# Kernel tuning notes

Hardware: AMD Instinct MI355X
Metric: run time of the kernel (lower is better)

The kernel has to match this reference:

```python
import jax, jax.numpy as jnp
import numpy as np

LN_EPS = 1e-5  # torch nn.LayerNorm default


def setup_inputs() -> dict:
    key = jax.random.key(0)
    kx, kw = jax.random.split(key)
    T, B, D = 1024, 8, 2048
    x = jax.random.normal(kx, (T, B, D), dtype=jnp.float32)
    c0 = jnp.zeros((B, D), dtype=jnp.float32)
    # Linear(n_embd, 3*n_embd, bias=False) weight: [3D, D], scaled for sane activations
    W = jax.random.normal(kw, (3 * D, D), dtype=jnp.float32) / np.sqrt(D)
    gamma = jnp.ones((D,), dtype=jnp.float32)
    beta = jnp.zeros((D,), dtype=jnp.float32)
    return {"x": x, "c0": c0, "W": W, "gamma": gamma, "beta": beta}


def reference(x, c0, W, gamma, beta):
    # x: [T, B, D], c0: [B, D], W: [3D, D]
    T, B, D = x.shape
    # Projection for all timesteps at once (same math as per-step Linear).
    ufr = jnp.einsum('tbd,ed->tbe', x, W)  # [T, B, 3D]
    u, f, r = jnp.split(ufr, 3, axis=-1)
    f = jax.nn.sigmoid(f)
    r = jax.nn.sigmoid(r)

    def step(c_prev, inp):
        x_t, u_t, f_t, r_t = inp
        c_t = f_t * c_prev + (1.0 - f_t) * u_t
        h_t = r_t * jnp.tanh(c_t) + (1.0 - r_t) * x_t
        return c_t, h_t

    c_T, h = jax.lax.scan(step, c0, (x, u, f, r))  # h: [T, B, D]

    g = jax.nn.gelu(h, approximate=False)  # torch F.gelu default = exact erf
    mean = jnp.mean(g, axis=-1, keepdims=True)
    var = jnp.var(g, axis=-1, keepdims=True)
    out = (g - mean) * jax.lax.rsqrt(var + LN_EPS) * gamma + beta
    return out, c_T
```

## Files before the change

kernel.cpp:

```cpp
#include <hip/hip_runtime.h>
#include <hip/hip_bf16.h>

#define T_DIM 1024
#define B_DIM 8
#define D_DIM 2048
#define E_DIM 6144
#define N_ROWS 8192
#define K_DIM 2048
#define LN_EPS 1e-5f

#define S2  128
#define CH2 8
#define BD (B_DIM * D_DIM)

typedef short bf16x8 __attribute__((ext_vector_type(8)));
typedef float f32x4 __attribute__((ext_vector_type(4)));

__device__ __forceinline__ unsigned short f2bf(float f) {
  unsigned u = __float_as_uint(f);
  u += 0x7fffu + ((u >> 16) & 1u);
  return (unsigned short)(u >> 16);
}
__device__ __forceinline__ float bf2f(unsigned short h) {
  return __uint_as_float(((unsigned)h) << 16);
}
__device__ __forceinline__ float fast_sigmoid(float x) {
  return __builtin_amdgcn_rcpf(1.f + __expf(-x));
}
__device__ __forceinline__ float fast_tanh(float x) {
  return 1.f - 2.f * __builtin_amdgcn_rcpf(__expf(2.f * x) + 1.f);
}

__global__ __launch_bounds__(256) void cvt2_kernel(
    const float* __restrict__ src0, unsigned short* __restrict__ dst0, int n0,
    const float* __restrict__ src1, unsigned short* __restrict__ dst1, int n1) {
  int i = blockIdx.x * 256 + threadIdx.x;
  const float* s;
  unsigned short* d;
  if (i < n0) {
    s = src0; d = dst0;
  } else {
    i -= n0;
    if (i >= n1) return;
    s = src1; d = dst1;
  }
  float4 v = reinterpret_cast<const float4*>(s)[i];
  ushort4 o;
  o.x = f2bf(v.x); o.y = f2bf(v.y); o.z = f2bf(v.z); o.w = f2bf(v.w);
  reinterpret_cast<ushort4*>(d)[i] = o;
}

#define NT2 32

__global__ __launch_bounds__(512, 2) void gemm8_kernel(
    const unsigned short* __restrict__ A,
    const unsigned short* __restrict__ Bw,
    unsigned short* __restrict__ C) {
  extern __shared__ __align__(16) char smem[];
  const int tid  = threadIdx.x;
  const int lane = tid & 63;
  const int wave = tid >> 6;
  const int wm = wave >> 2;
  const int wn = wave & 3;

  const int bid = blockIdx.x;
  const int tileM = ((bid & 7) * 4 + ((bid >> 3) & 3)) * 256;
  const int tileN = (bid >> 5) * 256;

  const int p0i = wave * 2048 + lane * 16;
  const int p1i = p0i + 1024;
  const int q0i = p0i ^ (((p0i >> 9) & 1) << 5);
  const int q1i = p1i ^ (((p1i >> 9) & 1) << 5);
  const int go0 = ((q0i >> 6) & 127) * 4096 + ((q0i >> 13) << 6) + (q0i & 63);
  const int go1 = ((q1i >> 6) & 127) * 4096 + ((q1i >> 13) << 6) + (q1i & 63);
  const char* Ab = (const char*)A + (size_t)tileM * 4096;
  const char* Bb = (const char*)Bw + (size_t)tileN * 4096;

#define STAGE(kt, h, bufOff)                                                 \
  {                                                                          \
    const char* gs_ = ((h) < 2 ? Ab : Bb) +                                  \
                      (size_t)(((h) & 1) * 128) * 4096 + (size_t)(kt) * 128; \
    char* ds_ = smem + (bufOff) + (h) * 16384 + wave * 2048;                 \
    __builtin_amdgcn_global_load_lds(                                        \
        (const __attribute__((address_space(1))) void*)(gs_ + go0),          \
        (__attribute__((address_space(3))) void*)ds_, 16, 0, 0);             \
    __builtin_amdgcn_global_load_lds(                                        \
        (const __attribute__((address_space(1))) void*)(gs_ + go1),          \
        (__attribute__((address_space(3))) void*)(ds_ + 1024), 16, 0, 0);    \
  }

  const int xbit = ((lane >> 3) & 1) << 5;
  const int aBase = wm * 16384 +
                    (((lane & 15) * 64 + (lane >> 4) * 16) ^ xbit);
  const int bBase = 32768 + (wn >> 1) * 16384 +
                    ((((wn & 1) * 64 + (lane & 15)) * 64 + (lane >> 4) * 16) ^ xbit);

#define RDA(m, bufOff)                                                          \
  a[m][0] = *reinterpret_cast<const bf16x8*>(smem + (bufOff) + aBase + (m) * 1024);        \
  a[m][1] = *reinterpret_cast<const bf16x8*>(smem + (bufOff) + aBase + (m) * 1024 + 8192);
#define RDB(n, bufOff)                                                          \
  b[n][0] = *reinterpret_cast<const bf16x8*>(smem + (bufOff) + bBase + (n) * 1024);        \
  b[n][1] = *reinterpret_cast<const bf16x8*>(smem + (bufOff) + bBase + (n) * 1024 + 8192);
#define MM(m, n)                                                                \
  acc[m][n] = __builtin_amdgcn_mfma_f32_16x16x32_bf16(a[m][0], b[n][0], acc[m][n], 0, 0, 0); \
  acc[m][n] = __builtin_amdgcn_mfma_f32_16x16x32_bf16(a[m][1], b[n][1], acc[m][n], 0, 0, 0);

  bf16x8 a[8][2], b[4][2];
  f32x4 acc[8][4] = {};

  STAGE(0, 0, 0); STAGE(0, 1, 0); STAGE(0, 2, 0); STAGE(0, 3, 0);
  STAGE(1, 0, 65536); STAGE(1, 1, 65536);
  asm volatile("s_waitcnt vmcnt(4)" ::: "memory");
  __builtin_amdgcn_s_barrier();
  RDA(0, 0); RDA(1, 0); RDA(2, 0); RDA(3, 0);
  RDB(0, 0); RDB(1, 0);

  for (int j = 0; j < NT2; ++j) {
    const int buf  = (j & 1) << 16;
    const int nbuf = buf ^ 65536;
    asm volatile("s_waitcnt lgkmcnt(0)" ::: "memory");
    __builtin_amdgcn_s_setprio(1);
    if (j < NT2 - 1) STAGE(j + 1, 2, nbuf);
    RDA(4, buf); RDA(5, buf); RDA(6, buf); RDA(7, buf);
    MM(0, 0); MM(0, 1); MM(1, 0); MM(1, 1);
    MM(2, 0); MM(2, 1); MM(3, 0); MM(3, 1);
    __builtin_amdgcn_s_setprio(0);
    __builtin_amdgcn_s_barrier();
    asm volatile("s_waitcnt lgkmcnt(0)" ::: "memory");
    __builtin_amdgcn_s_setprio(1);
    if (j < NT2 - 1) STAGE(j + 1, 3, nbuf);
    RDB(2, buf); RDB(3, buf);
    MM(4, 0); MM(4, 1); MM(5, 0); MM(5, 1);
    MM(6, 0); MM(6, 1); MM(7, 0); MM(7, 1);
    __builtin_amdgcn_s_setprio(0);
    __builtin_amdgcn_s_barrier();
    asm volatile("s_waitcnt lgkmcnt(0)" ::: "memory");
    __builtin_amdgcn_s_setprio(1);
    if (j < NT2 - 2) STAGE(j + 2, 0, buf);
    MM(0, 2); MM(0, 3); MM(1, 2); MM(1, 3);
    MM(2, 2); MM(2, 3); MM(3, 2); MM(3, 3);
    __builtin_amdgcn_s_setprio(0);
    __builtin_amdgcn_s_barrier();
    if (j < NT2 - 2) {
      STAGE(j + 2, 1, buf);
      asm volatile("s_waitcnt vmcnt(4)" ::: "memory");
    } else if (j == NT2 - 2) {
      asm volatile("s_waitcnt vmcnt(0)" ::: "memory");
    }
    __builtin_amdgcn_s_barrier();
    __builtin_amdgcn_s_setprio(1);
    RDA(0, nbuf); RDA(1, nbuf); RDA(2, nbuf); RDA(3, nbuf);
    RDB(0, nbuf); RDB(1, nbuf);
    MM(4, 2); MM(4, 3); MM(5, 2); MM(5, 3);
    MM(6, 2); MM(6, 3); MM(7, 2); MM(7, 3);
    __builtin_amdgcn_s_setprio(0);
    __builtin_amdgcn_s_barrier();
  }

  const int crow = (lane >> 4) * 4;
  const int ccol = lane & 15;
#pragma unroll
  for (int m = 0; m < 8; ++m) {
#pragma unroll
    for (int n = 0; n < 4; ++n) {
#pragma unroll
      for (int jj = 0; jj < 4; ++jj) {
        int row = tileM + wm * 128 + m * 16 + crow + jj;
        int col = tileN + wn * 64 + n * 16 + ccol;
        C[(size_t)row * E_DIM + col] = f2bf(acc[m][n][jj]);
      }
    }
  }
#undef STAGE
#undef RDA
#undef RDB
#undef MM
}

__global__ __launch_bounds__(256) void scan_p1_kernel(
    const unsigned short* __restrict__ ufr,
    unsigned short* __restrict__ Aout, unsigned short* __restrict__ Bout) {
  const int idx4 = blockIdx.x * 256 + threadIdx.x;
  const int s = blockIdx.y;
  const int b = idx4 >> 9;
  const int d = (idx4 & 511) * 4;
  const unsigned short* up =
      ufr + ((size_t)(s * CH2) * B_DIM + b) * E_DIM + d;
  float A0 = 1.f, A1 = 1.f, A2 = 1.f, A3 = 1.f;
  float Bv0 = 0.f, Bv1 = 0.f, Bv2 = 0.f, Bv3 = 0.f;
#pragma unroll
  for (int it = 0; it < CH2; ++it) {
    ushort4 uv = *(const ushort4*)up;
    ushort4 fv = *(const ushort4*)(up + D_DIM);
    float f0 = fast_sigmoid(bf2f(fv.x));
    float f1 = fast_sigmoid(bf2f(fv.y));
    float f2 = fast_sigmoid(bf2f(fv.z));
    float f3 = fast_sigmoid(bf2f(fv.w));
    A0 *= f0; Bv0 = f0 * Bv0 + (1.f - f0) * bf2f(uv.x);
    A1 *= f1; Bv1 = f1 * Bv1 + (1.f - f1) * bf2f(uv.y);
    A2 *= f2; Bv2 = f2 * Bv2 + (1.f - f2) * bf2f(uv.z);
    A3 *= f3; Bv3 = f3 * Bv3 + (1.f - f3) * bf2f(uv.w);
    up += (size_t)B_DIM * E_DIM;
  }
  size_t o = (size_t)s * BD + b * D_DIM + d;
  ushort4 ao = {f2bf(A0), f2bf(A1), f2bf(A2), f2bf(A3)};
  ushort4 bo = {f2bf(Bv0), f2bf(Bv1), f2bf(Bv2), f2bf(Bv3)};
  *(ushort4*)(Aout + o) = ao;
  *(ushort4*)(Bout + o) = bo;
}

__global__ __launch_bounds__(64) void scan_p2_kernel(
    const float* __restrict__ c0,
    const unsigned short* __restrict__ Ain, const unsigned short* __restrict__ Bin,
    unsigned short* __restrict__ cs, float* __restrict__ cT) {
  const int idx = blockIdx.x * 64 + threadIdx.x;
  float c = c0[idx];
  for (int s = 0; s < S2; ++s) {
    cs[(size_t)s * BD + idx] = f2bf(c);
    c = bf2f(Ain[(size_t)s * BD + idx]) * c + bf2f(Bin[(size_t)s * BD + idx]);
  }
  cT[idx] = c;
}

__global__ __launch_bounds__(256) void scan_p3ln_kernel(
    const unsigned short* __restrict__ xb,
    const unsigned short* __restrict__ ufr,
    const unsigned short* __restrict__ csb,
    const float* __restrict__ gamma,
    const float* __restrict__ beta,
    float* __restrict__ out) {
  const int b = blockIdx.x & (B_DIM - 1);
  const int s = blockIdx.x >> 3;
  const int tid = threadIdx.x;
  const int lane = tid & 63;
  const int wave = tid >> 6;
  const int d0 = tid * 8;
  __shared__ float red[8];

  float c[8];
  {
    const unsigned short* csp = csb + (size_t)s * BD + b * D_DIM + d0;
    ushort4 v0 = *(const ushort4*)csp;
    ushort4 v1 = *(const ushort4*)(csp + 4);
    c[0]=bf2f(v0.x); c[1]=bf2f(v0.y); c[2]=bf2f(v0.z); c[3]=bf2f(v0.w);
    c[4]=bf2f(v1.x); c[5]=bf2f(v1.y); c[6]=bf2f(v1.z); c[7]=bf2f(v1.w);
  }
  float gam[8], bet[8];
  {
    float4 g0 = *(const float4*)(gamma + d0);
    float4 g1 = *(const float4*)(gamma + d0 + 4);
    float4 b0 = *(const float4*)(beta + d0);
    float4 b1 = *(const float4*)(beta + d0 + 4);
    gam[0]=g0.x; gam[1]=g0.y; gam[2]=g0.z; gam[3]=g0.w;
    gam[4]=g1.x; gam[5]=g1.y; gam[6]=g1.z; gam[7]=g1.w;
    bet[0]=b0.x; bet[1]=b0.y; bet[2]=b0.z; bet[3]=b0.w;
    bet[4]=b1.x; bet[5]=b1.y; bet[6]=b1.z; bet[7]=b1.w;
  }

  for (int it = 0; it < CH2; ++it) {
    const size_t rowo = (size_t)(s * CH2 + it) * B_DIM + b;
    const unsigned short* up = ufr + rowo * E_DIM + d0;
    const unsigned short* xp = xb + rowo * D_DIM + d0;
    ushort4 uv0 = *(const ushort4*)up;
    ushort4 uv1 = *(const ushort4*)(up + 4);
    ushort4 fv0 = *(const ushort4*)(up + D_DIM);
    ushort4 fv1 = *(const ushort4*)(up + D_DIM + 4);
    ushort4 rv0 = *(const ushort4*)(up + 2 * D_DIM);
    ushort4 rv1 = *(const ushort4*)(up + 2 * D_DIM + 4);
    ushort4 xv0 = *(const ushort4*)xp;
    ushort4 xv1 = *(const ushort4*)(xp + 4);
    unsigned short uu[8] = {uv0.x, uv0.y, uv0.z, uv0.w, uv1.x, uv1.y, uv1.z, uv1.w};
    unsigned short ff[8] = {fv0.x, fv0.y, fv0.z, fv0.w, fv1.x, fv1.y, fv1.z, fv1.w};
    unsigned short rr[8] = {rv0.x, rv0.y, rv0.z, rv0.w, rv1.x, rv1.y, rv1.z, rv1.w};
    unsigned short xx[8] = {xv0.x, xv0.y, xv0.z, xv0.w, xv1.x, xv1.y, xv1.z, xv1.w};

    float g[8];
    float s1 = 0.f, sq = 0.f;
#pragma unroll
    for (int jj = 0; jj < 8; ++jj) {
      float f = fast_sigmoid(bf2f(ff[jj]));
      float r = fast_sigmoid(bf2f(rr[jj]));
      c[jj] = f * c[jj] + (1.f - f) * bf2f(uu[jj]);
      float h = r * fast_tanh(c[jj]) + (1.f - r) * bf2f(xx[jj]);
      float gg = 0.5f * h * (1.f + erff(h * 0.70710678118654752f));
      g[jj] = gg;
      s1 += gg;
      sq += gg * gg;
    }
#pragma unroll
    for (int off = 32; off; off >>= 1) {
      s1 += __shfl_xor(s1, off);
      sq += __shfl_xor(sq, off);
    }
    if (lane == 0) { red[wave] = s1; red[4 + wave] = sq; }
    __syncthreads();
    float S1 = red[0] + red[1] + red[2] + red[3];
    float Sq = red[4] + red[5] + red[6] + red[7];
    __syncthreads();
    float mean = S1 * (1.f / D_DIM);
    float var  = Sq * (1.f / D_DIM) - mean * mean;
    float inv = rsqrtf(var + LN_EPS);

    float* op = out + rowo * D_DIM + d0;
    float4 o0 = {(g[0] - mean) * inv * gam[0] + bet[0],
                 (g[1] - mean) * inv * gam[1] + bet[1],
                 (g[2] - mean) * inv * gam[2] + bet[2],
                 (g[3] - mean) * inv * gam[3] + bet[3]};
    float4 o1 = {(g[4] - mean) * inv * gam[4] + bet[4],
                 (g[5] - mean) * inv * gam[5] + bet[5],
                 (g[6] - mean) * inv * gam[6] + bet[6],
                 (g[7] - mean) * inv * gam[7] + bet[7]};
    *(float4*)op = o0;
    *(float4*)(op + 4) = o1;
  }
}

extern "C" void kernel_launch(void* const* d_in, const int* in_sizes, int n_in,
                              void* d_out, int out_size, void* d_ws, size_t ws_size,
                              hipStream_t stream) {
  const float* x     = (const float*)d_in[0];
  const float* c0    = (const float*)d_in[1];
  const float* W     = (const float*)d_in[2];
  const float* gamma = (const float*)d_in[3];
  const float* beta  = (const float*)d_in[4];
  float* out = (float*)d_out;
  float* cT  = out + (size_t)N_ROWS * D_DIM;

  unsigned short* ufr = (unsigned short*)d_ws;
  unsigned short* xb  = ufr + (size_t)N_ROWS * E_DIM;
  unsigned short* wb  = xb + (size_t)N_ROWS * K_DIM;

  unsigned short* Abuf = wb;
  unsigned short* Bbuf = Abuf + (size_t)S2 * BD;
  unsigned short* csb  = Bbuf + (size_t)S2 * BD;

  int nx4 = N_ROWS * K_DIM / 4;
  int nw4 = E_DIM * K_DIM / 4;
  cvt2_kernel<<<(nx4 + nw4 + 255) / 256, 256, 0, stream>>>(x, xb, nx4, W, wb, nw4);

  (void)hipFuncSetAttribute((const void*)gemm8_kernel,
                            hipFuncAttributeMaxDynamicSharedMemorySize, 131072);
  gemm8_kernel<<<768, 512, 131072, stream>>>(xb, wb, ufr);

  dim3 sg(BD / 4 / 256, S2);
  scan_p1_kernel<<<sg, 256, 0, stream>>>(ufr, Abuf, Bbuf);
  scan_p2_kernel<<<BD / 64, 64, 0, stream>>>(c0, Abuf, Bbuf, csb, cT);
  scan_p3ln_kernel<<<B_DIM * S2, 256, 0, stream>>>(xb, ufr, csb, gamma, beta, out);
}
```

Baseline: 266.9 us.

## Widen memory accesses to 16-byte vectors and software-pipeline scan pass-2 loads

```diff
diff --git a/kernel.cpp b/kernel.cpp
--- a/kernel.cpp
+++ b/kernel.cpp
@@ -14,6 +14,7 @@
 #define BD (B_DIM * D_DIM)
 
 typedef short bf16x8 __attribute__((ext_vector_type(8)));
+typedef unsigned short u16x8 __attribute__((ext_vector_type(8)));
 typedef float f32x4 __attribute__((ext_vector_type(4)));
 
 __device__ __forceinline__ unsigned short f2bf(float f) {
@@ -44,10 +45,12 @@
     if (i >= n1) return;
     s = src1; d = dst1;
   }
-  float4 v = reinterpret_cast<const float4*>(s)[i];
-  ushort4 o;
-  o.x = f2bf(v.x); o.y = f2bf(v.y); o.z = f2bf(v.z); o.w = f2bf(v.w);
-  reinterpret_cast<ushort4*>(d)[i] = o;
+  float4 v0 = reinterpret_cast<const float4*>(s)[i * 2];
+  float4 v1 = reinterpret_cast<const float4*>(s)[i * 2 + 1];
+  u16x8 o;
+  o[0] = f2bf(v0.x); o[1] = f2bf(v0.y); o[2] = f2bf(v0.z); o[3] = f2bf(v0.w);
+  o[4] = f2bf(v1.x); o[5] = f2bf(v1.y); o[6] = f2bf(v1.z); o[7] = f2bf(v1.w);
+  *reinterpret_cast<u16x8*>(d + (size_t)i * 8) = o;
 }
 
 #define NT2 32
@@ -180,33 +183,33 @@
 __global__ __launch_bounds__(256) void scan_p1_kernel(
     const unsigned short* __restrict__ ufr,
     unsigned short* __restrict__ Aout, unsigned short* __restrict__ Bout) {
-  const int idx4 = blockIdx.x * 256 + threadIdx.x;
+  const int idx8 = blockIdx.x * 256 + threadIdx.x;
   const int s = blockIdx.y;
-  const int b = idx4 >> 9;
-  const int d = (idx4 & 511) * 4;
+  const int b = idx8 >> 8;
+  const int d = (idx8 & 255) * 8;
   const unsigned short* up =
       ufr + ((size_t)(s * CH2) * B_DIM + b) * E_DIM + d;
-  float A0 = 1.f, A1 = 1.f, A2 = 1.f, A3 = 1.f;
-  float Bv0 = 0.f, Bv1 = 0.f, Bv2 = 0.f, Bv3 = 0.f;
+  float Av[8], Bv[8];
+#pragma unroll
+  for (int q = 0; q < 8; ++q) { Av[q] = 1.f; Bv[q] = 0.f; }
 #pragma unroll
   for (int it = 0; it < CH2; ++it) {
-    ushort4 uv = *(const ushort4*)up;
-    ushort4 fv = *(const ushort4*)(up + D_DIM);
-    float f0 = fast_sigmoid(bf2f(fv.x));
-    float f1 = fast_sigmoid(bf2f(fv.y));
-    float f2 = fast_sigmoid(bf2f(fv.z));
-    float f3 = fast_sigmoid(bf2f(fv.w));
-    A0 *= f0; Bv0 = f0 * Bv0 + (1.f - f0) * bf2f(uv.x);
-    A1 *= f1; Bv1 = f1 * Bv1 + (1.f - f1) * bf2f(uv.y);
-    A2 *= f2; Bv2 = f2 * Bv2 + (1.f - f2) * bf2f(uv.z);
-    A3 *= f3; Bv3 = f3 * Bv3 + (1.f - f3) * bf2f(uv.w);
+    u16x8 uv = *reinterpret_cast<const u16x8*>(up);
+    u16x8 fv = *reinterpret_cast<const u16x8*>(up + D_DIM);
+#pragma unroll
+    for (int q = 0; q < 8; ++q) {
+      float f = fast_sigmoid(bf2f(fv[q]));
+      Av[q] *= f;
+      Bv[q] = f * Bv[q] + (1.f - f) * bf2f(uv[q]);
+    }
     up += (size_t)B_DIM * E_DIM;
   }
   size_t o = (size_t)s * BD + b * D_DIM + d;
-  ushort4 ao = {f2bf(A0), f2bf(A1), f2bf(A2), f2bf(A3)};
-  ushort4 bo = {f2bf(Bv0), f2bf(Bv1), f2bf(Bv2), f2bf(Bv3)};
-  *(ushort4*)(Aout + o) = ao;
-  *(ushort4*)(Bout + o) = bo;
+  u16x8 ao, bo;
+#pragma unroll
+  for (int q = 0; q < 8; ++q) { ao[q] = f2bf(Av[q]); bo[q] = f2bf(Bv[q]); }
+  *reinterpret_cast<u16x8*>(Aout + o) = ao;
+  *reinterpret_cast<u16x8*>(Bout + o) = bo;
 }
 
 __global__ __launch_bounds__(64) void scan_p2_kernel(
@@ -215,10 +218,28 @@
     unsigned short* __restrict__ cs, float* __restrict__ cT) {
   const int idx = blockIdx.x * 64 + threadIdx.x;
   float c = c0[idx];
-  for (int s = 0; s < S2; ++s) {
-    cs[(size_t)s * BD + idx] = f2bf(c);
-    c = bf2f(Ain[(size_t)s * BD + idx]) * c + bf2f(Bin[(size_t)s * BD + idx]);
-  }
+  unsigned short aP[8], bP[8], aQ[8], bQ[8];
+#define LOADB(AA, BB, sb)                                          \
+  _Pragma("unroll")                                                \
+  for (int q = 0; q < 8; ++q) {                                    \
+    AA[q] = Ain[(size_t)((sb) + q) * BD + idx];                    \
+    BB[q] = Bin[(size_t)((sb) + q) * BD + idx];                    \
+  }
+#define COMPB(AA, BB, sb)                                          \
+  _Pragma("unroll")                                                \
+  for (int q = 0; q < 8; ++q) {                                    \
+    cs[(size_t)((sb) + q) * BD + idx] = f2bf(c);                   \
+    c = bf2f(AA[q]) * c + bf2f(BB[q]);                             \
+  }
+  LOADB(aP, bP, 0);
+  for (int sb = 0; sb < S2; sb += 16) {
+    LOADB(aQ, bQ, sb + 8);
+    COMPB(aP, bP, sb);
+    if (sb + 16 < S2) { LOADB(aP, bP, sb + 16); }
+    COMPB(aQ, bQ, sb + 8);
+  }
+#undef LOADB
+#undef COMPB
   cT[idx] = c;
 }
 
@@ -239,11 +260,9 @@
 
   float c[8];
   {
-    const unsigned short* csp = csb + (size_t)s * BD + b * D_DIM + d0;
-    ushort4 v0 = *(const ushort4*)csp;
-    ushort4 v1 = *(const ushort4*)(csp + 4);
-    c[0]=bf2f(v0.x); c[1]=bf2f(v0.y); c[2]=bf2f(v0.z); c[3]=bf2f(v0.w);
-    c[4]=bf2f(v1.x); c[5]=bf2f(v1.y); c[6]=bf2f(v1.z); c[7]=bf2f(v1.w);
+    u16x8 v = *reinterpret_cast<const u16x8*>(csb + (size_t)s * BD + b * D_DIM + d0);
+#pragma unroll
+    for (int q = 0; q < 8; ++q) c[q] = bf2f(v[q]);
   }
   float gam[8], bet[8];
   {
@@ -260,28 +279,19 @@
   for (int it = 0; it < CH2; ++it) {
     const size_t rowo = (size_t)(s * CH2 + it) * B_DIM + b;
     const unsigned short* up = ufr + rowo * E_DIM + d0;
-    const unsigned short* xp = xb + rowo * D_DIM + d0;
-    ushort4 uv0 = *(const ushort4*)up;
-    ushort4 uv1 = *(const ushort4*)(up + 4);
-    ushort4 fv0 = *(const ushort4*)(up + D_DIM);
-    ushort4 fv1 = *(const ushort4*)(up + D_DIM + 4);
-    ushort4 rv0 = *(const ushort4*)(up + 2 * D_DIM);
-    ushort4 rv1 = *(const ushort4*)(up + 2 * D_DIM + 4);
-    ushort4 xv0 = *(const ushort4*)xp;
-    ushort4 xv1 = *(const ushort4*)(xp + 4);
-    unsigned short uu[8] = {uv0.x, uv0.y, uv0.z, uv0.w, uv1.x, uv1.y, uv1.z, uv1.w};
-    unsigned short ff[8] = {fv0.x, fv0.y, fv0.z, fv0.w, fv1.x, fv1.y, fv1.z, fv1.w};
-    unsigned short rr[8] = {rv0.x, rv0.y, rv0.z, rv0.w, rv1.x, rv1.y, rv1.z, rv1.w};
-    unsigned short xx[8] = {xv0.x, xv0.y, xv0.z, xv0.w, xv1.x, xv1.y, xv1.z, xv1.w};
+    u16x8 uv = *reinterpret_cast<const u16x8*>(up);
+    u16x8 fv = *reinterpret_cast<const u16x8*>(up + D_DIM);
+    u16x8 rv = *reinterpret_cast<const u16x8*>(up + 2 * D_DIM);
+    u16x8 xv = *reinterpret_cast<const u16x8*>(xb + rowo * D_DIM + d0);
 
     float g[8];
     float s1 = 0.f, sq = 0.f;
 #pragma unroll
     for (int jj = 0; jj < 8; ++jj) {
-      float f = fast_sigmoid(bf2f(ff[jj]));
-      float r = fast_sigmoid(bf2f(rr[jj]));
-      c[jj] = f * c[jj] + (1.f - f) * bf2f(uu[jj]);
-      float h = r * fast_tanh(c[jj]) + (1.f - r) * bf2f(xx[jj]);
+      float f = fast_sigmoid(bf2f(fv[jj]));
+      float r = fast_sigmoid(bf2f(rv[jj]));
+      c[jj] = f * c[jj] + (1.f - f) * bf2f(uv[jj]);
+      float h = r * fast_tanh(c[jj]) + (1.f - r) * bf2f(xv[jj]);
       float gg = 0.5f * h * (1.f + erff(h * 0.70710678118654752f));
       g[jj] = gg;
       s1 += gg;
@@ -334,15 +344,15 @@
   unsigned short* Bbuf = Abuf + (size_t)S2 * BD;
   unsigned short* csb  = Bbuf + (size_t)S2 * BD;
 
-  int nx4 = N_ROWS * K_DIM / 4;
-  int nw4 = E_DIM * K_DIM / 4;
-  cvt2_kernel<<<(nx4 + nw4 + 255) / 256, 256, 0, stream>>>(x, xb, nx4, W, wb, nw4);
+  int nx8 = N_ROWS * K_DIM / 8;
+  int nw8 = E_DIM * K_DIM / 8;
+  cvt2_kernel<<<(nx8 + nw8 + 255) / 256, 256, 0, stream>>>(x, xb, nx8, W, wb, nw8);
 
   (void)hipFuncSetAttribute((const void*)gemm8_kernel,
                             hipFuncAttributeMaxDynamicSharedMemorySize, 131072);
   gemm8_kernel<<<768, 512, 131072, stream>>>(xb, wb, ufr);
 
-  dim3 sg(BD / 4 / 256, S2);
+  dim3 sg(BD / 8 / 256, S2);
   scan_p1_kernel<<<sg, 256, 0, stream>>>(ufr, Abuf, Bbuf);
   scan_p2_kernel<<<BD / 64, 64, 0, stream>>>(c0, Abuf, Bbuf, csb, cT);
   scan_p3ln_kernel<<<B_DIM * S2, 256, 0, stream>>>(xb, ufr, csb, gamma, beta, out);
```

After: 264.4 us. About the same (-0.9%).
